# Optimization experiments

Hardware: AMD Instinct MI355X
Metric: run time of the kernel (lower is better)

Reference implementation:

```python
import jax, jax.numpy as jnp
import numpy as np

K_NEIGHBORS = 16
NUM_PATCHES = 32
W_NORMAL = 1.0
W_SURFVAR = 1.0


def _knn_centered(points, k):
    """points: [B, N, 3] -> k nearest neighbors re-centered at each point, [B, N, k, 3].
    Distances are computed on stop_gradient(points) to match torch's .detach()."""
    pd = jax.lax.stop_gradient(points)
    # squared pairwise distances [B, N, N] (sqrt is monotone -> topk order identical)
    d2 = jnp.sum((pd[:, :, None, :] - pd[:, None, :, :]) ** 2, axis=-1)
    _, idx = jax.lax.top_k(-d2, k)  # smallest-k indices, [B, N, k]
    knn = jax.vmap(lambda pts, id_: pts[id_])(points, idx)  # [B, N, k, 3]
    return knn - points[:, :, None, :]


def _eig_props(knn):
    """knn: [B, N, k, 3] -> (normal [B,N,3] = eigvec of smallest eigval, eigvals [B,N,3] ascending)."""
    cov = jnp.einsum('bnki,bnkj->bnij', knn, knn)  # [B, N, 3, 3]
    w, v = jnp.linalg.eigh(cov)  # ascending eigenvalues, matches torch.symeig
    return v[..., :, 0], w


def setup_inputs() -> dict:
    key = jax.random.key(0)
    pointCloud = jax.random.normal(key, (4, 8192, 3), dtype=jnp.float32)
    return {"pointCloud": pointCloud}


def reference(pointCloud):
    B, N, _ = pointCloud.shape
    pp = N // NUM_PATCHES

    # global kNN / normals / surface variance
    knn_g = _knn_centered(pointCloud, K_NEIGHBORS)
    nrm_g, w_g = _eig_props(knn_g)

    # patchwise: each patch is an independent small point cloud -> fold patches into batch
    patch_pts = pointCloud.reshape(B * NUM_PATCHES, pp, 3)
    knn_p = _knn_centered(patch_pts, K_NEIGHBORS)
    nrm_p, w_p = _eig_props(knn_p)
    nrm_p = nrm_p.reshape(B, N, 3)

    # normal loss (abs variant, sign-ambiguity-free)
    loss_n = jnp.mean(jnp.linalg.norm(jnp.abs(nrm_p) - jnp.abs(nrm_g), axis=2)) * W_NORMAL

    # surface variance loss: lambda_min / sum(lambda)
    sv_g = w_g[..., 0] / jnp.sum(w_g, axis=-1)            # [B, N]
    sv_p = (w_p[..., 0] / jnp.sum(w_p, axis=-1)).reshape(B, N)
    loss_sv = jnp.mean((sv_p - sv_g) ** 2) * W_SURFVAR

    return jnp.stack([loss_n, loss_sv])  # [2] (original returns list of two [1] tensors)
```

## Files before the change

kernel.cpp:

```cpp
#include <hip/hip_runtime.h>
#include <math.h>

#define KNN 16
#define NPTS 8192
#define PTCH 256
#define NPATCH 32
#define NBATCH 4
#define NQ 32
#define SSTRIDE 130
#define LAMBDA_T 64.0f

#define NC 16
#define NCELLS (NC * NC * NC)
#define GMIN -4.2f
#define ICS 1.9047619f

__global__ void zero2_kernel(float* out) { out[0] = 0.0f; out[1] = 0.0f; }

__device__ __forceinline__ float lam_f(float r, float s)
{
    const float C     = 0.063493636f;
    const float SQ2PI = 2.5066283f;
    const float IS2   = 0.70710678f;
    float a = fabsf(r - s), b = r + s;
    float amr = a - r;
    float coefA = amr * amr + 2.f - s * s;
    float I = 2.f * __expf(-0.5f * b * b) - coefA * __expf(-0.5f * a * a)
            + r * SQ2PI * (erff(b * IS2) - erff(a * IS2));
    float M = C * (3.14159265f / r) * I;
    if (s > r) {
        float u = s - r;
        M += 12.566371f * C * (1.2533141f * erff(u * IS2) - u * __expf(-0.5f * u * u));
    }
    return (float)NPTS * M;
}

__device__ __forceinline__ void jrot(double& app, double& aqq, double& apq,
                                     double& arp, double& arq,
                                     double& vp0, double& vq0,
                                     double& vp1, double& vq1,
                                     double& vp2, double& vq2)
{
    double g = apq;
    if (g == 0.0) return;
    double theta = (aqq - app) / (2.0 * g);
    double at = fabs(theta);
    double t = (at > 1.0e154) ? (0.5 / theta)
                              : (copysign(1.0, theta) / (at + sqrt(theta * theta + 1.0)));
    double c = 1.0 / sqrt(t * t + 1.0);
    double s = t * c;
    double tau = s / (1.0 + c);
    app -= t * g;
    aqq += t * g;
    apq = 0.0;
    double rp = arp, rq = arq;
    arp = rp - s * (rq + tau * rp);
    arq = rq + s * (rp - tau * rq);
    double p0 = vp0, q0 = vq0;
    vp0 = p0 - s * (q0 + tau * p0); vq0 = q0 + s * (p0 - tau * q0);
    double p1 = vp1, q1 = vq1;
    vp1 = p1 - s * (q1 + tau * p1); vq1 = q1 + s * (p1 - tau * q1);
    double p2 = vp2, q2 = vq2;
    vp2 = p2 - s * (q2 + tau * p2); vq2 = q2 + s * (p2 - tau * q2);
}

__device__ __forceinline__ void eig3(double a00, double a11, double a22,
                                     double a01, double a02, double a12,
                                     double& nx, double& ny, double& nz,
                                     double& lmin, double& lsum)
{
    double v00 = 1, v01 = 0, v02 = 0;
    double v10 = 0, v11 = 1, v12 = 0;
    double v20 = 0, v21 = 0, v22 = 1;
    double scale = fabs(a00) + fabs(a11) + fabs(a22) + fabs(a01) + fabs(a02) + fabs(a12);
    if (scale > 0.0) {
        for (int sweep = 0; sweep < 6; ++sweep) {
            double off = fabs(a01) + fabs(a02) + fabs(a12);
            if (off <= scale * 1e-15) break;
            jrot(a00, a11, a01, a02, a12, v00, v01, v10, v11, v20, v21);
            jrot(a00, a22, a02, a01, a12, v00, v02, v10, v12, v20, v22);
            jrot(a11, a22, a12, a01, a02, v01, v02, v11, v12, v21, v22);
        }
    }
    lsum = a00 + a11 + a22;
    lmin = a00; nx = v00; ny = v10; nz = v20;
    if (a11 < lmin) { lmin = a11; nx = v01; ny = v11; nz = v21; }
    if (a22 < lmin) { lmin = a22; nx = v02; ny = v12; nz = v22; }
}

__device__ __forceinline__ unsigned mkkey(float d2, unsigned idx) {
    return (__float_as_uint(d2) & 0xFFFFE000u) | idx;
}

__device__ __forceinline__ void insert16(unsigned key, unsigned* L)
{
    L[KNN - 1] = key;
    #pragma unroll
    for (int m = KNN - 1; m >= 1; --m) {
        unsigned a = L[m - 1], b = L[m];
        L[m - 1] = min(a, b);
        L[m]     = max(a, b);
    }
}

__device__ __forceinline__ void merge4(unsigned* L, int lane)
{
    #pragma unroll
    for (int step = 1; step <= 2; step <<= 1) {
        unsigned tmp[KNN];
        #pragma unroll
        for (int m = 0; m < KNN; ++m) tmp[m] = __shfl(L[m], lane ^ step, 64);
        for (int m = 0; m < KNN; ++m) {
            if (tmp[m] >= L[KNN - 1]) break;
            insert16(tmp[m], L);
        }
    }
}

__device__ __forceinline__ float rfl(float x) {
    return __int_as_float(__builtin_amdgcn_readfirstlane(__float_as_int(x)));
}
__device__ __forceinline__ unsigned mbcnt64(unsigned long long m) {
    return __builtin_amdgcn_mbcnt_hi((unsigned)(m >> 32),
           __builtin_amdgcn_mbcnt_lo((unsigned)m, 0u));
}

__device__ __forceinline__ int cidx(float v) {
    int i = (int)floorf((v - GMIN) * ICS);
    return min(max(i, 0), NC - 1);
}
__device__ __forceinline__ int cellOf(float x, float y, float z) {
    return (cidx(z) * NC + cidx(y)) * NC + cidx(x);
}

__global__ void __launch_bounds__(256) count_kernel(const float* __restrict__ pts,
                                                    unsigned* __restrict__ counts)
{
    int gid = blockIdx.x * 256 + threadIdx.x;
    int b = gid >> 13, i = gid & (NPTS - 1);
    const float* p = pts + (size_t)b * (NPTS * 3) + (size_t)i * 3;
    atomicAdd(&counts[b * NCELLS + cellOf(p[0], p[1], p[2])], 1u);
}

__global__ void __launch_bounds__(256) scan_kernel(const unsigned* __restrict__ counts,
                                                   unsigned* __restrict__ cellStart,
                                                   unsigned* __restrict__ cellPos)
{
    __shared__ unsigned part[256];
    const int b = blockIdx.x, t = threadIdx.x;
    const unsigned* cnt = counts + b * NCELLS;
    unsigned loc[16], s = 0;
    #pragma unroll
    for (int i = 0; i < 16; ++i) { loc[i] = s; s += cnt[t * 16 + i]; }
    part[t] = s;
    __syncthreads();
    for (int o = 1; o < 256; o <<= 1) {
        unsigned u = (t >= o) ? part[t - o] : 0u;
        __syncthreads();
        part[t] += u;
        __syncthreads();
    }
    unsigned base = part[t] - s;
    unsigned* csb = cellStart + b * (NCELLS + 1);
    unsigned* cpb = cellPos + b * NCELLS;
    #pragma unroll
    for (int i = 0; i < 16; ++i) {
        unsigned e = base + loc[i];
        csb[t * 16 + i] = e;
        cpb[t * 16 + i] = e;
    }
    if (t == 255) csb[NCELLS] = base + s;
}

__global__ void __launch_bounds__(256) scatter_kernel(const float* __restrict__ pts,
                                                      unsigned* __restrict__ cellPos,
                                                      float4* __restrict__ sorted)
{
    int gid = blockIdx.x * 256 + threadIdx.x;
    int b = gid >> 13, i = gid & (NPTS - 1);
    const float* p = pts + (size_t)b * (NPTS * 3) + (size_t)i * 3;
    float x = p[0], y = p[1], z = p[2];
    int c = cellOf(x, y, z);
    unsigned slot = atomicAdd(&cellPos[b * NCELLS + c], 1u);
    float4 v;
    v.x = x; v.y = y; v.z = z; v.w = __uint_as_float((unsigned)i);
    sorted[(size_t)b * NPTS + slot] = v;
}

__global__ void __launch_bounds__(256, 4)
spl_main(const float* __restrict__ pts, float* __restrict__ out,
         const unsigned* __restrict__ cellStart, const float4* __restrict__ sortedp)
{
    __shared__ float4 pbuf4[PTCH];
    __shared__ unsigned survk[NQ * SSTRIDE];
    __shared__ unsigned cnts[NQ];
    __shared__ float gbuf[NQ];
    __shared__ double xbuf[NQ * 4];
    __shared__ double rb[4];

    const int t = threadIdx.x;
    const int w = t >> 6;
    const int lane = t & 63;
    const int p = blockIdx.x;
    const int eighth = blockIdx.y;
    const int b = blockIdx.z;

    const float* base = pts + (size_t)b * (NPTS * 3);
    const int qbase = p * PTCH + eighth * NQ;
    const unsigned* cs = cellStart + b * (NCELLS + 1);
    const float4* sp = sortedp + (size_t)b * NPTS;

    {
        const float* src = base + p * (PTCH * 3);
        float* dst = (float*)pbuf4;
        #pragma unroll
        for (int s = 0; s < 3; ++s) {
            int f = t + s * 256;
            int j = f / 3;
            int c = f - 3 * j;
            dst[j * 4 + c] = src[f];
        }
    }
    if (t < NQ) {
        int qi = qbase + t;
        float x = base[qi * 3 + 0], y = base[qi * 3 + 1], z = base[qi * 3 + 2];
        float r = fmaxf(sqrtf(x * x + y * y + z * z), 0.01f);
        float lo = 0.f, hi = 12.f;
        #pragma unroll 1
        for (int it = 0; it < 16; ++it) {
            float mid = 0.5f * (lo + hi);
            if (lam_f(r, mid) < LAMBDA_T) lo = mid; else hi = mid;
        }
        gbuf[t] = hi * hi;
    }
    __syncthreads();

    #pragma unroll 1
    for (int u = 0; u < 8; ++u) {
        const int q = w * 8 + u;
        float4 qv = pbuf4[eighth * NQ + q];
        float qx = rfl(qv.x), qy = rfl(qv.y), qz = rfl(qv.z);
        float g2 = rfl(gbuf[q]);
        float g = sqrtf(g2);
        int ixlo = cidx(qx - g), ixhi = cidx(qx + g);
        int iylo = cidx(qy - g), iyhi = cidx(qy + g);
        int izlo = cidx(qz - g), izhi = cidx(qz + g);
        int nx = ixhi - ixlo + 1;
        int ny = iyhi - iylo + 1;
        int nyz = ny * (izhi - izlo + 1);
        unsigned cnt = 0;
        unsigned sbase = (unsigned)q * SSTRIDE;
        #pragma unroll 1
        for (int r0 = 0; r0 < nyz; r0 += 64) {
            int r = r0 + lane;
            unsigned sB = 0, eB = 0;
            if (r < nyz) {
                int iz = izlo + r / ny;
                int iy = iylo + (r - (r / ny) * ny);
                int cb = (iz * NC + iy) * NC + ixlo;
                sB = cs[cb];
                eB = cs[cb + nx];
            }
            int rmax = min(nyz - r0, 64);
            #pragma unroll 1
            for (int rr = 0; rr < rmax; ++rr) {
                unsigned s0 = __shfl(sB, rr);
                unsigned e0 = __shfl(eB, rr);
                #pragma unroll 1
                for (unsigned jb = s0; jb < e0; jb += 64) {
                    unsigned j = jb + (unsigned)lane;
                    bool in = j < e0;
                    float4 c = sp[min(j, e0 - 1u)];
                    float dx = qx - c.x, dy = qy - c.y, dz = qz - c.z;
                    float d2 = dx * dx + dy * dy + dz * dz;
                    bool pass = in && (d2 < g2);
                    unsigned long long m = __ballot(pass);
                    if (m) {
                        if (pass) {
                            unsigned slot = min(cnt + mbcnt64(m), (unsigned)(SSTRIDE - 1));
                            survk[sbase + slot] = mkkey(d2, __float_as_uint(c.w));
                        }
                        cnt += (unsigned)__popcll(m);
                    }
                }
            }
        }
        if (lane == 0) cnts[q] = cnt;
    }
    __syncthreads();

    const int qq = lane >> 2;
    const int h = lane & 3;
    const int myq = (w & 1) * 16 + qq;
    float4 qv = pbuf4[eighth * NQ + myq];
    const float pqx = qv.x, pqy = qv.y, pqz = qv.z;

    double ngx = 0, ngy = 0, ngz = 0, svg = 0;

    if (w < 2) {
        unsigned gl[KNN];
        #pragma unroll
        for (int m = 0; m < KNN; ++m) gl[m] = 0xFFFFFFFFu;
        unsigned cnt = cnts[myq];
        bool valid = (cnt >= KNN) && (cnt <= SSTRIDE);
        if (valid) {
            unsigned share = (cnt + 3) >> 2;
            unsigned m0 = h * share;
            unsigned m1 = min(m0 + share, cnt);
            #pragma unroll 1
            for (unsigned m = m0; m < m1; ++m) {
                unsigned k = survk[myq * SSTRIDE + m];
                if (k < gl[KNN - 1]) insert16(k, gl);
            }
        }
        merge4(gl, lane);
        if (valid) {
            float g = gbuf[myq];
            float upper = __uint_as_float((gl[KNN - 1] & 0xFFFFE000u) + 0x2000u);
            valid = (upper < g * 0.999f - 1e-5f);
        }
        if (__any((h == 0 && !valid) ? 1 : 0)) {
            if (h == 0 && !valid) {
                #pragma unroll
                for (int m = 0; m < KNN; ++m) gl[m] = 0xFFFFFFFFu;
                #pragma unroll 1
                for (int i = 0; i < NPTS; ++i) {
                    float cx = base[i * 3 + 0];
                    float cy = base[i * 3 + 1];
                    float cz = base[i * 3 + 2];
                    float dx = pqx - cx, dy = pqy - cy, dz = pqz - cz;
                    float d2 = dx * dx + dy * dy + dz * dz;
                    unsigned k = mkkey(d2, (unsigned)i);
                    if (k < gl[KNN - 1]) insert16(k, gl);
                }
            }
        }
        if (h == 0) {
            double c00 = 0, c11 = 0, c22 = 0, c01 = 0, c02 = 0, c12 = 0;
            const double qxd = pqx, qyd = pqy, qzd = pqz;
            #pragma unroll
            for (int m = 0; m < KNN; ++m) {
                int idx = (int)(gl[m] & 0x1FFFu);
                double dx = (double)base[idx * 3 + 0] - qxd;
                double dy = (double)base[idx * 3 + 1] - qyd;
                double dz = (double)base[idx * 3 + 2] - qzd;
                c00 += dx * dx; c11 += dy * dy; c22 += dz * dz;
                c01 += dx * dy; c02 += dx * dz; c12 += dy * dz;
            }
            double lmin, lsum;
            eig3(c00, c11, c22, c01, c02, c12, ngx, ngy, ngz, lmin, lsum);
            svg = lmin / lsum;
        }
    } else {
        unsigned pl[KNN];
        #pragma unroll
        for (int m = 0; m < KNN; ++m) pl[m] = 0xFFFFFFFFu;
        const int j0 = h * 64;
        #pragma unroll 1
        for (int j = j0; j < j0 + 64; ++j) {
            float4 c = pbuf4[j];
            float dx = pqx - c.x, dy = pqy - c.y, dz = pqz - c.z;
            float d2 = dx * dx + dy * dy + dz * dz;
            unsigned k = mkkey(d2, (unsigned)j);
            if (k < pl[KNN - 1]) insert16(k, pl);
        }
        merge4(pl, lane);
        if (h == 0) {
            double c00 = 0, c11 = 0, c22 = 0, c01 = 0, c02 = 0, c12 = 0;
            const double qxd = pqx, qyd = pqy, qzd = pqz;
            #pragma unroll
            for (int m = 0; m < KNN; ++m) {
                int idx = (int)(pl[m] & 0x1FFFu);
                float4 cpt = pbuf4[idx];
                double dx = (double)cpt.x - qxd;
                double dy = (double)cpt.y - qyd;
                double dz = (double)cpt.z - qzd;
                c00 += dx * dx; c11 += dy * dy; c22 += dz * dz;
                c01 += dx * dy; c02 += dx * dz; c12 += dy * dz;
            }
            double nx, ny, nz, lmin, lsum;
            eig3(c00, c11, c22, c01, c02, c12, nx, ny, nz, lmin, lsum);
            xbuf[myq * 4 + 0] = nx;
            xbuf[myq * 4 + 1] = ny;
            xbuf[myq * 4 + 2] = nz;
            xbuf[myq * 4 + 3] = lmin / lsum;
        }
    }
    __syncthreads();

    double ln = 0.0, lsv = 0.0;
    if (w < 2 && h == 0) {
        double npx = xbuf[myq * 4 + 0];
        double npy = xbuf[myq * 4 + 1];
        double npz = xbuf[myq * 4 + 2];
        double svp = xbuf[myq * 4 + 3];
        double dx = fabs(npx) - fabs(ngx);
        double dy = fabs(npy) - fabs(ngy);
        double dz = fabs(npz) - fabs(ngz);
        ln  = sqrt(dx * dx + dy * dy + dz * dz);
        double ds = svp - svg;
        lsv = ds * ds;
    }
    if (w < 2) {
        #pragma unroll
        for (int o = 32; o > 0; o >>= 1) {
            ln  += __shfl_down(ln, o);
            lsv += __shfl_down(lsv, o);
        }
        if (lane == 0) { rb[w * 2 + 0] = ln; rb[w * 2 + 1] = lsv; }
    }
    __syncthreads();
    if (t == 0) {
        const double inv = 1.0 / (double)(NBATCH * NPTS);
        atomicAdd(&out[0], (float)((rb[0] + rb[2]) * inv));
        atomicAdd(&out[1], (float)((rb[1] + rb[3]) * inv));
    }
}

extern "C" void kernel_launch(void* const* d_in, const int* in_sizes, int n_in,
                              void* d_out, int out_size, void* d_ws, size_t ws_size,
                              hipStream_t stream)
{
    const float* pts = (const float*)d_in[0];
    float* out = (float*)d_out;

    unsigned char* ws = (unsigned char*)d_ws;
    unsigned* counts    = (unsigned*)(ws);
    unsigned* cellStart = (unsigned*)(ws + 65536);
    unsigned* cellPos   = (unsigned*)(ws + 131088);
    float4*   sorted    = (float4*)  (ws + 196624);

    hipLaunchKernelGGL(zero2_kernel, dim3(1), dim3(1), 0, stream, out);
    hipMemsetAsync(counts, 0, (size_t)NBATCH * NCELLS * sizeof(unsigned), stream);
    hipLaunchKernelGGL(count_kernel, dim3(NBATCH * NPTS / 256), dim3(256), 0, stream,
                       pts, counts);
    hipLaunchKernelGGL(scan_kernel, dim3(NBATCH), dim3(256), 0, stream,
                       counts, cellStart, cellPos);
    hipLaunchKernelGGL(scatter_kernel, dim3(NBATCH * NPTS / 256), dim3(256), 0, stream,
                       pts, cellPos, sorted);
    dim3 grid(NPATCH, 8, NBATCH);
    hipLaunchKernelGGL(spl_main, grid, dim3(256), 0, stream, pts, out, cellStart, sorted);
}
```

Baseline: 166.2 us.

## Fuse grid build into one kernel and halve queries per block

The zero, memset, count, scan and scatter launches are replaced by a single per-batch build_kernel. It does a shared-memory histogram, block scan and scatter, so four launches and the global atomics go away. The main kernel now handles 16 queries per block over twice as many blocks, with a higher occupancy hint, and unrolls the cell-row loop by 2. The build now runs on only 4 blocks, which serializes that phase, and half of the waves sit idle in the final kNN stage.

Measured after the change: 170.0 us. 1.02x slower.

```diff
diff --git a/kernel.cpp b/kernel.cpp
--- a/kernel.cpp
+++ b/kernel.cpp
@@ -6,7 +6,7 @@
 #define PTCH 256
 #define NPATCH 32
 #define NBATCH 4
-#define NQ 32
+#define NQ 16
 #define SSTRIDE 130
 #define LAMBDA_T 64.0f
 
@@ -14,8 +14,6 @@
 #define NCELLS (NC * NC * NC)
 #define GMIN -4.2f
 #define ICS 1.9047619f
-
-__global__ void zero2_kernel(float* out) { out[0] = 0.0f; out[1] = 0.0f; }
 
 __device__ __forceinline__ float lam_f(float r, float s)
 {
@@ -133,61 +131,64 @@
     return (cidx(z) * NC + cidx(y)) * NC + cidx(x);
 }
 
-__global__ void __launch_bounds__(256) count_kernel(const float* __restrict__ pts,
-                                                    unsigned* __restrict__ counts)
-{
-    int gid = blockIdx.x * 256 + threadIdx.x;
-    int b = gid >> 13, i = gid & (NPTS - 1);
-    const float* p = pts + (size_t)b * (NPTS * 3) + (size_t)i * 3;
-    atomicAdd(&counts[b * NCELLS + cellOf(p[0], p[1], p[2])], 1u);
-}
-
-__global__ void __launch_bounds__(256) scan_kernel(const unsigned* __restrict__ counts,
-                                                   unsigned* __restrict__ cellStart,
-                                                   unsigned* __restrict__ cellPos)
-{
-    __shared__ unsigned part[256];
-    const int b = blockIdx.x, t = threadIdx.x;
-    const unsigned* cnt = counts + b * NCELLS;
-    unsigned loc[16], s = 0;
-    #pragma unroll
-    for (int i = 0; i < 16; ++i) { loc[i] = s; s += cnt[t * 16 + i]; }
+#define BT 1024
+__global__ void __launch_bounds__(1024)
+build_kernel(const float* __restrict__ pts, float* __restrict__ out,
+             unsigned* __restrict__ cellStart, float4* __restrict__ sorted)
+{
+    __shared__ unsigned hist[NCELLS];
+    __shared__ unsigned part[BT];
+    const int b = blockIdx.x;
+    const int t = threadIdx.x;
+    if (b == 0 && t == 0) { out[0] = 0.0f; out[1] = 0.0f; }
+    for (int i = t; i < NCELLS; i += BT) hist[i] = 0u;
+    __syncthreads();
+    const float* base = pts + (size_t)b * (NPTS * 3);
+    float px[8], py[8], pz[8];
+    int pc[8];
+    #pragma unroll
+    for (int k = 0; k < 8; ++k) {
+        int i = k * BT + t;
+        px[k] = base[i * 3 + 0];
+        py[k] = base[i * 3 + 1];
+        pz[k] = base[i * 3 + 2];
+        pc[k] = cellOf(px[k], py[k], pz[k]);
+        atomicAdd(&hist[pc[k]], 1u);
+    }
+    __syncthreads();
+    unsigned loc[4], s = 0;
+    #pragma unroll
+    for (int i = 0; i < 4; ++i) { loc[i] = s; s += hist[t * 4 + i]; }
     part[t] = s;
     __syncthreads();
-    for (int o = 1; o < 256; o <<= 1) {
+    for (int o = 1; o < BT; o <<= 1) {
         unsigned u = (t >= o) ? part[t - o] : 0u;
         __syncthreads();
         part[t] += u;
         __syncthreads();
     }
-    unsigned base = part[t] - s;
+    unsigned basex = part[t] - s;
     unsigned* csb = cellStart + b * (NCELLS + 1);
-    unsigned* cpb = cellPos + b * NCELLS;
-    #pragma unroll
-    for (int i = 0; i < 16; ++i) {
-        unsigned e = base + loc[i];
-        csb[t * 16 + i] = e;
-        cpb[t * 16 + i] = e;
-    }
-    if (t == 255) csb[NCELLS] = base + s;
-}
-
-__global__ void __launch_bounds__(256) scatter_kernel(const float* __restrict__ pts,
-                                                      unsigned* __restrict__ cellPos,
-                                                      float4* __restrict__ sorted)
-{
-    int gid = blockIdx.x * 256 + threadIdx.x;
-    int b = gid >> 13, i = gid & (NPTS - 1);
-    const float* p = pts + (size_t)b * (NPTS * 3) + (size_t)i * 3;
-    float x = p[0], y = p[1], z = p[2];
-    int c = cellOf(x, y, z);
-    unsigned slot = atomicAdd(&cellPos[b * NCELLS + c], 1u);
-    float4 v;
-    v.x = x; v.y = y; v.z = z; v.w = __uint_as_float((unsigned)i);
-    sorted[(size_t)b * NPTS + slot] = v;
-}
-
-__global__ void __launch_bounds__(256, 4)
+    #pragma unroll
+    for (int i = 0; i < 4; ++i) {
+        unsigned e = basex + loc[i];
+        csb[t * 4 + i] = e;
+        hist[t * 4 + i] = e;
+    }
+    if (t == BT - 1) csb[NCELLS] = basex + s;
+    __syncthreads();
+    float4* sb = sorted + (size_t)b * NPTS;
+    #pragma unroll
+    for (int k = 0; k < 8; ++k) {
+        int i = k * BT + t;
+        unsigned slot = atomicAdd(&hist[pc[k]], 1u);
+        float4 v;
+        v.x = px[k]; v.y = py[k]; v.z = pz[k]; v.w = __uint_as_float((unsigned)i);
+        sb[slot] = v;
+    }
+}
+
+__global__ void __launch_bounds__(256, 8)
 spl_main(const float* __restrict__ pts, float* __restrict__ out,
          const unsigned* __restrict__ cellStart, const float4* __restrict__ sortedp)
 {
@@ -196,17 +197,16 @@
     __shared__ unsigned cnts[NQ];
     __shared__ float gbuf[NQ];
     __shared__ double xbuf[NQ * 4];
-    __shared__ double rb[4];
 
     const int t = threadIdx.x;
     const int w = t >> 6;
     const int lane = t & 63;
     const int p = blockIdx.x;
-    const int eighth = blockIdx.y;
+    const int sixt = blockIdx.y;
     const int b = blockIdx.z;
 
     const float* base = pts + (size_t)b * (NPTS * 3);
-    const int qbase = p * PTCH + eighth * NQ;
+    const int qbase = p * PTCH + sixt * NQ;
     const unsigned* cs = cellStart + b * (NCELLS + 1);
     const float4* sp = sortedp + (size_t)b * NPTS;
 
@@ -236,9 +236,9 @@
     __syncthreads();
 
     #pragma unroll 1
-    for (int u = 0; u < 8; ++u) {
-        const int q = w * 8 + u;
-        float4 qv = pbuf4[eighth * NQ + q];
+    for (int u = 0; u < 4; ++u) {
+        const int q = w * 4 + u;
+        float4 qv = pbuf4[sixt * NQ + q];
         float qx = rfl(qv.x), qy = rfl(qv.y), qz = rfl(qv.z);
         float g2 = rfl(gbuf[q]);
         float g = sqrtf(g2);
@@ -262,7 +262,7 @@
                 eB = cs[cb + nx];
             }
             int rmax = min(nyz - r0, 64);
-            #pragma unroll 1
+            #pragma unroll 2
             for (int rr = 0; rr < rmax; ++rr) {
                 unsigned s0 = __shfl(sB, rr);
                 unsigned e0 = __shfl(eB, rr);
@@ -291,13 +291,13 @@
 
     const int qq = lane >> 2;
     const int h = lane & 3;
-    const int myq = (w & 1) * 16 + qq;
-    float4 qv = pbuf4[eighth * NQ + myq];
+    const int myq = qq;
+    float4 qv = pbuf4[sixt * NQ + myq];
     const float pqx = qv.x, pqy = qv.y, pqz = qv.z;
 
     double ngx = 0, ngy = 0, ngz = 0, svg = 0;
 
-    if (w < 2) {
+    if (w == 0) {
         unsigned gl[KNN];
         #pragma unroll
         for (int m = 0; m < KNN; ++m) gl[m] = 0xFFFFFFFFu;
@@ -351,7 +351,7 @@
             eig3(c00, c11, c22, c01, c02, c12, ngx, ngy, ngz, lmin, lsum);
             svg = lmin / lsum;
         }
-    } else {
+    } else if (w == 1) {
         unsigned pl[KNN];
         #pragma unroll
         for (int m = 0; m < KNN; ++m) pl[m] = 0xFFFFFFFFu;
@@ -388,32 +388,30 @@
     }
     __syncthreads();
 
-    double ln = 0.0, lsv = 0.0;
-    if (w < 2 && h == 0) {
-        double npx = xbuf[myq * 4 + 0];
-        double npy = xbuf[myq * 4 + 1];
-        double npz = xbuf[myq * 4 + 2];
-        double svp = xbuf[myq * 4 + 3];
-        double dx = fabs(npx) - fabs(ngx);
-        double dy = fabs(npy) - fabs(ngy);
-        double dz = fabs(npz) - fabs(ngz);
-        ln  = sqrt(dx * dx + dy * dy + dz * dz);
-        double ds = svp - svg;
-        lsv = ds * ds;
-    }
-    if (w < 2) {
+    if (w == 0) {
+        double ln = 0.0, lsv = 0.0;
+        if (h == 0) {
+            double npx = xbuf[myq * 4 + 0];
+            double npy = xbuf[myq * 4 + 1];
+            double npz = xbuf[myq * 4 + 2];
+            double svp = xbuf[myq * 4 + 3];
+            double dx = fabs(npx) - fabs(ngx);
+            double dy = fabs(npy) - fabs(ngy);
+            double dz = fabs(npz) - fabs(ngz);
+            ln  = sqrt(dx * dx + dy * dy + dz * dz);
+            double ds = svp - svg;
+            lsv = ds * ds;
+        }
         #pragma unroll
         for (int o = 32; o > 0; o >>= 1) {
             ln  += __shfl_down(ln, o);
             lsv += __shfl_down(lsv, o);
         }
-        if (lane == 0) { rb[w * 2 + 0] = ln; rb[w * 2 + 1] = lsv; }
-    }
-    __syncthreads();
-    if (t == 0) {
-        const double inv = 1.0 / (double)(NBATCH * NPTS);
-        atomicAdd(&out[0], (float)((rb[0] + rb[2]) * inv));
-        atomicAdd(&out[1], (float)((rb[1] + rb[3]) * inv));
+        if (lane == 0) {
+            const double inv = 1.0 / (double)(NBATCH * NPTS);
+            atomicAdd(&out[0], (float)(ln * inv));
+            atomicAdd(&out[1], (float)(lsv * inv));
+        }
     }
 }
 
@@ -425,19 +423,11 @@
     float* out = (float*)d_out;
 
     unsigned char* ws = (unsigned char*)d_ws;
-    unsigned* counts    = (unsigned*)(ws);
-    unsigned* cellStart = (unsigned*)(ws + 65536);
-    unsigned* cellPos   = (unsigned*)(ws + 131088);
-    float4*   sorted    = (float4*)  (ws + 196624);
-
-    hipLaunchKernelGGL(zero2_kernel, dim3(1), dim3(1), 0, stream, out);
-    hipMemsetAsync(counts, 0, (size_t)NBATCH * NCELLS * sizeof(unsigned), stream);
-    hipLaunchKernelGGL(count_kernel, dim3(NBATCH * NPTS / 256), dim3(256), 0, stream,
-                       pts, counts);
-    hipLaunchKernelGGL(scan_kernel, dim3(NBATCH), dim3(256), 0, stream,
-                       counts, cellStart, cellPos);
-    hipLaunchKernelGGL(scatter_kernel, dim3(NBATCH * NPTS / 256), dim3(256), 0, stream,
-                       pts, cellPos, sorted);
-    dim3 grid(NPATCH, 8, NBATCH);
+    unsigned* cellStart = (unsigned*)(ws);
+    float4*   sorted    = (float4*)  (ws + 65552);
+
+    hipLaunchKernelGGL(build_kernel, dim3(NBATCH), dim3(BT), 0, stream,
+                       pts, out, cellStart, sorted);
+    dim3 grid(NPATCH, 16, NBATCH);
     hipLaunchKernelGGL(spl_main, grid, dim3(256), 0, stream, pts, out, cellStart, sorted);
 }
```
